# Kernel tuning notes

Hardware: AMD Instinct MI355X
Metric: run time of the kernel (lower is better)

## Reference

```python
import jax, jax.numpy as jnp
import numpy as np

B, T, J, C = 256, 100, 32, 3
EDGES = 101   # self.bins = bins + 1 edges
NBINS = EDGES - 1
EPS = 1e-08


def setup_inputs() -> dict:
    key = jax.random.key(0)
    k1, k2 = jax.random.split(key)
    data1 = jax.random.normal(k1, (B, T, J, C), dtype=jnp.float32)
    data2 = jax.random.normal(k2, (B, T, J, C), dtype=jnp.float32)
    return {"data1": data1, "data2": data2}


def _pairwise(d):
    # [B,T,J,C] -> [B,T,J,J] pairwise Euclidean distances over the joint axis
    diff = d[..., :, None, :] - d[..., None, :, :]
    return jnp.sqrt((diff * diff).sum(-1))


def _hist_density(x, edges):
    # x: [N] flat row, edges: [EDGES] sorted bin edges (torch.histogram semantics:
    # right-open bins, except the last bin which includes the right edge; density
    # normalizes by total count * bin width)
    idx = jnp.clip(jnp.searchsorted(edges, x, side='right') - 1, 0, NBINS - 1)
    counts = jnp.zeros(NBINS, dtype=x.dtype).at[idx].add(1.0)
    widths = jnp.diff(edges)
    return counts / (counts.sum() * widths)


def _entropy(px, qx):
    return (px * (jnp.log(px + EPS) - jnp.log(qx + EPS))).sum(1)


def reference(data1, data2):
    p1 = _pairwise(data1).reshape(data1.shape[0], -1)  # [B, T*J*J]
    p2 = _pairwise(data2).reshape(data2.shape[0], -1)
    both = jnp.concatenate([p1, p2], axis=1)
    mn = both.min(1)
    mx = both.max(1)
    # tensor_linspace: per-row uniform edges between row min and row max
    w0 = jnp.linspace(1.0, 0.0, EDGES, dtype=p1.dtype)
    w1 = jnp.linspace(0.0, 1.0, EDGES, dtype=p1.dtype)
    edges = mn[:, None] * w0 + mx[:, None] * w1  # [B, EDGES]
    px = jax.vmap(_hist_density)(p1, edges)  # [B, NBINS]
    qx = jax.vmap(_hist_density)(p2, edges)
    m = (px + qx) * 0.5
    return (_entropy(px, m) + _entropy(qx, m)) * 0.5  # [B]
```

## Files before the change

kernel.cpp:

```cpp
#include <hip/hip_runtime.h>

constexpr int BATCH       = 256;
constexpr int T           = 100;
constexpr int J           = 32;
constexpr int EDGES       = 101;
constexpr int NBINS       = 100;
constexpr int NPAIR       = (J * (J - 1)) / 2;
constexpr int PAIRS_TOTAL = T * NPAIR;
constexpr int NPOINTS     = T * J;
constexpr int ROW_FLOATS  = NPOINTS * 3;
constexpr int NREP        = 32;
constexpr int NTHREADS    = 1024;
constexpr int NWAVES      = NTHREADS / 64;
constexpr float EPSF      = 1e-8f;
constexpr float NTOT      = 102400.0f;

__device__ __forceinline__ float sqrt_approx(float s) {
    float r;
    asm("v_sqrt_f32 %0, %1" : "=v"(r) : "v"(s));
    return r;
}

__global__ __launch_bounds__(NTHREADS)
void jsd_kernel(const float* __restrict__ g1all,
                const float* __restrict__ g2all,
                float* __restrict__ out)
{
#pragma clang fp contract(off)
    __shared__ float2 spt[NPOINTS * 3];
    __shared__ unsigned int hist[2][NREP][EDGES];
    __shared__ unsigned int lut[NPAIR];
    __shared__ float edg[EDGES];
    __shared__ float sqe[EDGES];
    __shared__ float2 SQ2[NBINS];
    __shared__ float sred[NWAVES];
    __shared__ float sterm[NBINS];
    __shared__ float s_mx, s_invw;

    const int tid = threadIdx.x;
    const int row = blockIdx.x;
    const float* g1 = g1all + (size_t)row * ROW_FLOATS;
    const float* g2 = g2all + (size_t)row * ROW_FLOATS;

    for (int k = tid; k < NPOINTS; k += NTHREADS) {
        float x1 = g1[3 * k], y1 = g1[3 * k + 1], z1 = g1[3 * k + 2];
        float x2 = g2[3 * k], y2 = g2[3 * k + 1], z2 = g2[3 * k + 2];
        spt[3 * k + 0] = make_float2(x1, y1);
        spt[3 * k + 1] = make_float2(x2, y2);
        spt[3 * k + 2] = make_float2(z1, z2);
    }
    for (int k = tid; k < 2 * NREP * EDGES; k += NTHREADS)
        (&hist[0][0][0])[k] = 0u;
    if (tid < J) {
        const int a = tid;
        int p = a * (2 * J - a - 1) / 2;
        for (int c = a + 1; c < J; ++c)
            lut[p++] = (unsigned)(((a * 3) << 16) | (c * 3));
    }
    __syncthreads();

    float vmax = 0.0f;
    {
        int t0 = tid / NPAIR;
        int r  = tid - t0 * NPAIR;
        int tb = t0 * (J * 3);
        for (int p = tid; p < PAIRS_TOTAL; p += NTHREADS) {
            const unsigned e = lut[r];
            const int ia = tb + (int)(e >> 16);
            const int ib = tb + (int)(e & 0xffffu);
            float2 a0 = spt[ia], a1 = spt[ia + 1], a2 = spt[ia + 2];
            float2 b0 = spt[ib], b1 = spt[ib + 1], b2 = spt[ib + 2];
            float dx1 = a0.x - b0.x, dy1 = a0.y - b0.y, dz1 = a2.x - b2.x;
            float s1 = dx1 * dx1 + dy1 * dy1 + dz1 * dz1;
            float dx2 = a1.x - b1.x, dy2 = a1.y - b1.y, dz2 = a2.y - b2.y;
            float s2 = dx2 * dx2 + dy2 * dy2 + dz2 * dz2;
            vmax = fmaxf(vmax, fmaxf(s1, s2));
            r += 32;
            bool w = (r >= NPAIR);
            if (w) r -= NPAIR;
            tb += w ? (3 * J * 3) : (2 * J * 3);
        }
    }
    for (int off = 32; off > 0; off >>= 1)
        vmax = fmaxf(vmax, __shfl_down(vmax, off, 64));
    if ((tid & 63) == 0) sred[tid >> 6] = vmax;
    __syncthreads();
    if (tid == 0) {
        float m = sred[0];
        for (int w = 1; w < NWAVES; ++w) m = fmaxf(m, sred[w]);
        float mx = __fsqrt_rn(m);
        s_mx = mx;
        s_invw = 100.0f / mx;
    }
    __syncthreads();
    const float mx   = s_mx;
    const float invw = s_invw;

    if (tid < EDGES) {
        float w1 = (tid == EDGES - 1) ? 1.0f : ((float)tid * 0.01f);
        edg[tid] = mx * w1;
    }
    __syncthreads();

    if (tid < EDGES) {
        float e = edg[tid];
        float y = 0.0f;
        if (tid > 0) {
            y = __fmul_rn(e, e);
            for (int it = 0; it < 4 && __fsqrt_rn(y) < e; ++it)
                y = __int_as_float(__float_as_int(y) + 1);
            for (int it = 0; it < 8; ++it) {
                float py = __int_as_float(__float_as_int(y) - 1);
                if (__fsqrt_rn(py) >= e) y = py; else break;
            }
        }
        sqe[tid] = y;
    }
    __syncthreads();
    if (tid < NBINS) SQ2[tid] = make_float2(sqe[tid], sqe[tid + 1]);
    __syncthreads();

    const int rep = tid & (NREP - 1);
    unsigned int* __restrict__ h1 = &hist[0][rep][0];
    unsigned int* __restrict__ h2 = &hist[1][rep][0];
    {
        int t0 = tid / NPAIR;
        int r  = tid - t0 * NPAIR;
        int tb = t0 * (J * 3);
        for (int p = tid; p < PAIRS_TOTAL; p += NTHREADS) {
            const unsigned e = lut[r];
            const int ia = tb + (int)(e >> 16);
            const int ib = tb + (int)(e & 0xffffu);
            float2 a0 = spt[ia], a1 = spt[ia + 1], a2 = spt[ia + 2];
            float2 b0 = spt[ib], b1 = spt[ib + 1], b2 = spt[ib + 2];
            float dx1 = a0.x - b0.x, dy1 = a0.y - b0.y, dz1 = a2.x - b2.x;
            float s1 = dx1 * dx1 + dy1 * dy1 + dz1 * dz1;
            float dx2 = a1.x - b1.x, dy2 = a1.y - b1.y, dz2 = a2.y - b2.y;
            float s2 = dx2 * dx2 + dy2 * dy2 + dz2 * dz2;

            int i1 = (int)(sqrt_approx(s1) * invw);
            int i2 = (int)(sqrt_approx(s2) * invw);
            i1 = i1 < 0 ? 0 : (i1 > 99 ? 99 : i1);
            i2 = i2 < 0 ? 0 : (i2 > 99 ? 99 : i2);
            float2 t1 = SQ2[i1];
            float2 t2 = SQ2[i2];
            i1 += (s1 >= t1.y) ? 1 : 0;
            i1 -= (s1 <  t1.x) ? 1 : 0;
            i2 += (s2 >= t2.y) ? 1 : 0;
            i2 -= (s2 <  t2.x) ? 1 : 0;
            i1 = i1 > 99 ? 99 : i1;
            i2 = i2 > 99 ? 99 : i2;

            atomicAdd(&h1[i1], 2u);
            atomicAdd(&h2[i2], 2u);

            r += 32;
            bool w = (r >= NPAIR);
            if (w) r -= NPAIR;
            tb += w ? (3 * J * 3) : (2 * J * 3);
        }
    }
    __syncthreads();

    if (tid < NBINS) {
        unsigned int c1 = 0, c2 = 0;
        for (int rr = 0; rr < NREP; ++rr) { c1 += hist[0][rr][tid]; c2 += hist[1][rr][tid]; }
        if (tid == 0) { c1 += T * J; c2 += T * J; }

        float w   = edg[tid + 1] - edg[tid];
        float den = __fmul_rn(NTOT, w);
        float px  = __fdiv_rn((float)c1, den);
        float qx  = __fdiv_rn((float)c2, den);
        float m   = (px + qx) * 0.5f;
        float lm  = logf(m + EPSF);
        float term = px * (logf(px + EPSF) - lm) + qx * (logf(qx + EPSF) - lm);
        sterm[tid] = term;
    }
    __syncthreads();
    if (tid == 0) {
        float acc = 0.0f;
        for (int i = 0; i < NBINS; ++i) acc += sterm[i];
        out[row] = acc * 0.5f;
    }
}

extern "C" void kernel_launch(void* const* d_in, const int* in_sizes, int n_in,
                              void* d_out, int out_size, void* d_ws, size_t ws_size,
                              hipStream_t stream) {
    const float* d1 = (const float*)d_in[0];
    const float* d2 = (const float*)d_in[1];
    float* out = (float*)d_out;
    jsd_kernel<<<BATCH, NTHREADS, 0, stream>>>(d1, d2, out);
}
```

Measured before the change: 40.51 us.

## Restructure pairwise loop as circulant per-lane walk with register-held anchor joint

Replaces the LUT-indexed flat pair enumeration with a scheme where each lane owns one joint of a frame and walks offsets 1..16 cyclically. The offset-16 pairs are seen twice and get weight 1. The anchor joint's coordinates stay in registers and the LUT is removed. Shared memory uses a padded frame stride of 97 to reduce bank conflicts, and each lane's histogram replica is indexed by its joint. This is meant to cut LDS traffic and index arithmetic, at the cost of a tail pass for the last 4 frames and a fixed mapping of waves to frames.

```diff
diff --git a/kernel.cpp b/kernel.cpp
--- a/kernel.cpp
+++ b/kernel.cpp
@@ -1,19 +1,19 @@
 #include <hip/hip_runtime.h>
 
-constexpr int BATCH       = 256;
-constexpr int T           = 100;
-constexpr int J           = 32;
-constexpr int EDGES       = 101;
-constexpr int NBINS       = 100;
-constexpr int NPAIR       = (J * (J - 1)) / 2;
-constexpr int PAIRS_TOTAL = T * NPAIR;
-constexpr int NPOINTS     = T * J;
-constexpr int ROW_FLOATS  = NPOINTS * 3;
-constexpr int NREP        = 32;
-constexpr int NTHREADS    = 1024;
-constexpr int NWAVES      = NTHREADS / 64;
-constexpr float EPSF      = 1e-8f;
-constexpr float NTOT      = 102400.0f;
+constexpr int BATCH      = 256;
+constexpr int T          = 100;
+constexpr int J          = 32;
+constexpr int EDGES      = 101;
+constexpr int NBINS      = 100;
+constexpr int NPOINTS    = T * J;
+constexpr int ROW_FLOATS = NPOINTS * 3;
+constexpr int NREP       = 32;
+constexpr int NTHREADS   = 1024;
+constexpr int NWAVES     = NTHREADS / 64;
+constexpr int TSTRIDE    = 97;
+constexpr int TMAIN      = 96;
+constexpr float EPSF     = 1e-8f;
+constexpr float NTOT     = 102400.0f;
 
 __device__ __forceinline__ float sqrt_approx(float s) {
     float r;
@@ -27,9 +27,8 @@
                 float* __restrict__ out)
 {
 #pragma clang fp contract(off)
-    __shared__ float2 spt[NPOINTS * 3];
+    __shared__ float2 spt[T * TSTRIDE];
     __shared__ unsigned int hist[2][NREP][EDGES];
-    __shared__ unsigned int lut[NPAIR];
     __shared__ float edg[EDGES];
     __shared__ float sqe[EDGES];
     __shared__ float2 SQ2[NBINS];
@@ -37,53 +36,71 @@
     __shared__ float sterm[NBINS];
     __shared__ float s_mx, s_invw;
 
-    const int tid = threadIdx.x;
-    const int row = blockIdx.x;
+    const int tid  = threadIdx.x;
+    const int row  = blockIdx.x;
+    const int wid  = tid >> 6;
+    const int lane = tid & 63;
+    const int half = lane >> 5;
+    const int a    = lane & 31;
+    const int aoff = a * 3;
+
     const float* g1 = g1all + (size_t)row * ROW_FLOATS;
     const float* g2 = g2all + (size_t)row * ROW_FLOATS;
 
     for (int k = tid; k < NPOINTS; k += NTHREADS) {
         float x1 = g1[3 * k], y1 = g1[3 * k + 1], z1 = g1[3 * k + 2];
         float x2 = g2[3 * k], y2 = g2[3 * k + 1], z2 = g2[3 * k + 2];
-        spt[3 * k + 0] = make_float2(x1, y1);
-        spt[3 * k + 1] = make_float2(x2, y2);
-        spt[3 * k + 2] = make_float2(z1, z2);
+        const int base = (k >> 5) * TSTRIDE + (k & 31) * 3;
+        spt[base + 0] = make_float2(x1, y1);
+        spt[base + 1] = make_float2(x2, y2);
+        spt[base + 2] = make_float2(z1, z2);
     }
     for (int k = tid; k < 2 * NREP * EDGES; k += NTHREADS)
         (&hist[0][0][0])[k] = 0u;
-    if (tid < J) {
-        const int a = tid;
-        int p = a * (2 * J - a - 1) / 2;
-        for (int c = a + 1; c < J; ++c)
-            lut[p++] = (unsigned)(((a * 3) << 16) | (c * 3));
-    }
     __syncthreads();
 
     float vmax = 0.0f;
-    {
-        int t0 = tid / NPAIR;
-        int r  = tid - t0 * NPAIR;
-        int tb = t0 * (J * 3);
-        for (int p = tid; p < PAIRS_TOTAL; p += NTHREADS) {
-            const unsigned e = lut[r];
-            const int ia = tb + (int)(e >> 16);
-            const int ib = tb + (int)(e & 0xffffu);
-            float2 a0 = spt[ia], a1 = spt[ia + 1], a2 = spt[ia + 2];
-            float2 b0 = spt[ib], b1 = spt[ib + 1], b2 = spt[ib + 2];
-            float dx1 = a0.x - b0.x, dy1 = a0.y - b0.y, dz1 = a2.x - b2.x;
+    for (int r = 0; r < TMAIN / (NWAVES * 2); ++r) {
+        const int t    = r * (NWAVES * 2) + wid * 2 + half;
+        const int base = t * TSTRIDE;
+        const float2 o0 = spt[base + aoff];
+        const float2 o1 = spt[base + aoff + 1];
+        const float2 o2 = spt[base + aoff + 2];
+#pragma unroll 4
+        for (int k = 1; k <= 16; ++k) {
+            const int coff = base + ((a + k) & 31) * 3;
+            const float2 c0 = spt[coff];
+            const float2 c1 = spt[coff + 1];
+            const float2 c2 = spt[coff + 2];
+            float dx1 = o0.x - c0.x, dy1 = o0.y - c0.y, dz1 = o2.x - c2.x;
             float s1 = dx1 * dx1 + dy1 * dy1 + dz1 * dz1;
-            float dx2 = a1.x - b1.x, dy2 = a1.y - b1.y, dz2 = a2.y - b2.y;
+            float dx2 = o1.x - c1.x, dy2 = o1.y - c1.y, dz2 = o2.y - c2.y;
             float s2 = dx2 * dx2 + dy2 * dy2 + dz2 * dz2;
             vmax = fmaxf(vmax, fmaxf(s1, s2));
-            r += 32;
-            bool w = (r >= NPAIR);
-            if (w) r -= NPAIR;
-            tb += w ? (3 * J * 3) : (2 * J * 3);
         }
+    }
+#pragma unroll
+    for (int j = 0; j < 2; ++j) {
+        const int it   = wid * 4 + j * 2 + half;
+        const int t    = TMAIN + (it >> 4);
+        const int k    = (it & 15) + 1;
+        const int base = t * TSTRIDE;
+        const float2 o0 = spt[base + aoff];
+        const float2 o1 = spt[base + aoff + 1];
+        const float2 o2 = spt[base + aoff + 2];
+        const int coff = base + ((a + k) & 31) * 3;
+        const float2 c0 = spt[coff];
+        const float2 c1 = spt[coff + 1];
+        const float2 c2 = spt[coff + 2];
+        float dx1 = o0.x - c0.x, dy1 = o0.y - c0.y, dz1 = o2.x - c2.x;
+        float s1 = dx1 * dx1 + dy1 * dy1 + dz1 * dz1;
+        float dx2 = o1.x - c1.x, dy2 = o1.y - c1.y, dz2 = o2.y - c2.y;
+        float s2 = dx2 * dx2 + dy2 * dy2 + dz2 * dz2;
+        vmax = fmaxf(vmax, fmaxf(s1, s2));
     }
     for (int off = 32; off > 0; off >>= 1)
         vmax = fmaxf(vmax, __shfl_down(vmax, off, 64));
-    if ((tid & 63) == 0) sred[tid >> 6] = vmax;
+    if (lane == 0) sred[wid] = vmax;
     __syncthreads();
     if (tid == 0) {
         float m = sred[0];
@@ -93,12 +110,11 @@
         s_invw = 100.0f / mx;
     }
     __syncthreads();
-    const float mx   = s_mx;
     const float invw = s_invw;
 
     if (tid < EDGES) {
         float w1 = (tid == EDGES - 1) ? 1.0f : ((float)tid * 0.01f);
-        edg[tid] = mx * w1;
+        edg[tid] = s_mx * w1;
     }
     __syncthreads();
 
@@ -120,22 +136,23 @@
     if (tid < NBINS) SQ2[tid] = make_float2(sqe[tid], sqe[tid + 1]);
     __syncthreads();
 
-    const int rep = tid & (NREP - 1);
-    unsigned int* __restrict__ h1 = &hist[0][rep][0];
-    unsigned int* __restrict__ h2 = &hist[1][rep][0];
-    {
-        int t0 = tid / NPAIR;
-        int r  = tid - t0 * NPAIR;
-        int tb = t0 * (J * 3);
-        for (int p = tid; p < PAIRS_TOTAL; p += NTHREADS) {
-            const unsigned e = lut[r];
-            const int ia = tb + (int)(e >> 16);
-            const int ib = tb + (int)(e & 0xffffu);
-            float2 a0 = spt[ia], a1 = spt[ia + 1], a2 = spt[ia + 2];
-            float2 b0 = spt[ib], b1 = spt[ib + 1], b2 = spt[ib + 2];
-            float dx1 = a0.x - b0.x, dy1 = a0.y - b0.y, dz1 = a2.x - b2.x;
+    unsigned int* __restrict__ h1 = &hist[0][a][0];
+    unsigned int* __restrict__ h2 = &hist[1][a][0];
+    for (int r = 0; r < TMAIN / (NWAVES * 2); ++r) {
+        const int t    = r * (NWAVES * 2) + wid * 2 + half;
+        const int base = t * TSTRIDE;
+        const float2 o0 = spt[base + aoff];
+        const float2 o1 = spt[base + aoff + 1];
+        const float2 o2 = spt[base + aoff + 2];
+#pragma unroll 4
+        for (int k = 1; k <= 16; ++k) {
+            const int coff = base + ((a + k) & 31) * 3;
+            const float2 c0 = spt[coff];
+            const float2 c1 = spt[coff + 1];
+            const float2 c2 = spt[coff + 2];
+            float dx1 = o0.x - c0.x, dy1 = o0.y - c0.y, dz1 = o2.x - c2.x;
             float s1 = dx1 * dx1 + dy1 * dy1 + dz1 * dz1;
-            float dx2 = a1.x - b1.x, dy2 = a1.y - b1.y, dz2 = a2.y - b2.y;
+            float dx2 = o1.x - c1.x, dy2 = o1.y - c1.y, dz2 = o2.y - c2.y;
             float s2 = dx2 * dx2 + dy2 * dy2 + dz2 * dz2;
 
             int i1 = (int)(sqrt_approx(s1) * invw);
@@ -151,14 +168,45 @@
             i1 = i1 > 99 ? 99 : i1;
             i2 = i2 > 99 ? 99 : i2;
 
-            atomicAdd(&h1[i1], 2u);
-            atomicAdd(&h2[i2], 2u);
-
-            r += 32;
-            bool w = (r >= NPAIR);
-            if (w) r -= NPAIR;
-            tb += w ? (3 * J * 3) : (2 * J * 3);
+            const unsigned int wgt = (k < 16) ? 2u : 1u;
+            atomicAdd(&h1[i1], wgt);
+            atomicAdd(&h2[i2], wgt);
         }
+    }
+#pragma unroll
+    for (int j = 0; j < 2; ++j) {
+        const int it   = wid * 4 + j * 2 + half;
+        const int t    = TMAIN + (it >> 4);
+        const int k    = (it & 15) + 1;
+        const int base = t * TSTRIDE;
+        const float2 o0 = spt[base + aoff];
+        const float2 o1 = spt[base + aoff + 1];
+        const float2 o2 = spt[base + aoff + 2];
+        const int coff = base + ((a + k) & 31) * 3;
+        const float2 c0 = spt[coff];
+        const float2 c1 = spt[coff + 1];
+        const float2 c2 = spt[coff + 2];
+        float dx1 = o0.x - c0.x, dy1 = o0.y - c0.y, dz1 = o2.x - c2.x;
+        float s1 = dx1 * dx1 + dy1 * dy1 + dz1 * dz1;
+        float dx2 = o1.x - c1.x, dy2 = o1.y - c1.y, dz2 = o2.y - c2.y;
+        float s2 = dx2 * dx2 + dy2 * dy2 + dz2 * dz2;
+
+        int i1 = (int)(sqrt_approx(s1) * invw);
+        int i2 = (int)(sqrt_approx(s2) * invw);
+        i1 = i1 < 0 ? 0 : (i1 > 99 ? 99 : i1);
+        i2 = i2 < 0 ? 0 : (i2 > 99 ? 99 : i2);
+        float2 t1 = SQ2[i1];
+        float2 t2 = SQ2[i2];
+        i1 += (s1 >= t1.y) ? 1 : 0;
+        i1 -= (s1 <  t1.x) ? 1 : 0;
+        i2 += (s2 >= t2.y) ? 1 : 0;
+        i2 -= (s2 <  t2.x) ? 1 : 0;
+        i1 = i1 > 99 ? 99 : i1;
+        i2 = i2 > 99 ? 99 : i2;
+
+        const unsigned int wgt = (k < 16) ? 2u : 1u;
+        atomicAdd(&h1[i1], wgt);
+        atomicAdd(&h2[i2], wgt);
     }
     __syncthreads();
 
```

Measured after the change: 41.63 us. +2.8%, slower.

## Split JSD into max, histogram, and finalize kernels across time segments

Applied to the files above, without the earlier changes.

The single kernel that ran one 1024-thread block per batch row is split into three kernels. The first two each run 5 blocks per row (20 timesteps each), so the grid grows from 256 blocks to 1280. The max pass combines block results with a global atomicMax on the float bits. Partial histograms are summed into a global workspace with atomics, and a small third kernel computes the JSD. Pairs are now enumerated with a circular half-offset scheme that gives the diagonal-opposite pair weight 1, replacing the pair LUT. The design reloads the inputs twice and adds a memset and extra launches in exchange for more parallelism.

```diff
diff --git a/kernel.cpp b/kernel.cpp
--- a/kernel.cpp
+++ b/kernel.cpp
@@ -1,19 +1,21 @@
 #include <hip/hip_runtime.h>
 
-constexpr int BATCH       = 256;
-constexpr int T           = 100;
-constexpr int J           = 32;
-constexpr int EDGES       = 101;
-constexpr int NBINS       = 100;
-constexpr int NPAIR       = (J * (J - 1)) / 2;
-constexpr int PAIRS_TOTAL = T * NPAIR;
-constexpr int NPOINTS     = T * J;
-constexpr int ROW_FLOATS  = NPOINTS * 3;
-constexpr int NREP        = 32;
-constexpr int NTHREADS    = 1024;
-constexpr int NWAVES      = NTHREADS / 64;
-constexpr float EPSF      = 1e-8f;
-constexpr float NTOT      = 102400.0f;
+constexpr int BATCH      = 256;
+constexpr int T          = 100;
+constexpr int J          = 32;
+constexpr int EDGES      = 101;
+constexpr int NBINS      = 100;
+constexpr int ROW_FLOATS = T * J * 3;
+constexpr int TPB        = 20;
+constexpr int BPR        = 5;
+constexpr int NT1        = 640;
+constexpr int TSTRIDE    = 97;
+constexpr int NREP       = 32;
+constexpr float EPSF     = 1e-8f;
+constexpr float NTOT     = 102400.0f;
+
+constexpr size_t WS_HIST_OFF = 1024;
+constexpr size_t WS_BYTES    = WS_HIST_OFF + (size_t)BATCH * 2 * NBINS * sizeof(unsigned);
 
 __device__ __forceinline__ float sqrt_approx(float s) {
     float r;
@@ -21,65 +23,44 @@
     return r;
 }
 
-__global__ __launch_bounds__(NTHREADS)
-void jsd_kernel(const float* __restrict__ g1all,
-                const float* __restrict__ g2all,
-                float* __restrict__ out)
+__device__ __forceinline__ void stage_seg(float2* spt, const float* p1, const float* p2, int tid) {
+    const int t = tid >> 5, c = tid & 31;
+    const int base = t * TSTRIDE + c * 3;
+    spt[base + 0] = make_float2(p1[3 * tid],     p1[3 * tid + 1]);
+    spt[base + 1] = make_float2(p2[3 * tid],     p2[3 * tid + 1]);
+    spt[base + 2] = make_float2(p1[3 * tid + 2], p2[3 * tid + 2]);
+}
+
+__global__ __launch_bounds__(NT1)
+void k_max(const float* __restrict__ g1all, const float* __restrict__ g2all,
+           unsigned int* __restrict__ wmax)
 {
 #pragma clang fp contract(off)
-    __shared__ float2 spt[NPOINTS * 3];
-    __shared__ unsigned int hist[2][NREP][EDGES];
-    __shared__ unsigned int lut[NPAIR];
-    __shared__ float edg[EDGES];
-    __shared__ float sqe[EDGES];
-    __shared__ float2 SQ2[NBINS];
-    __shared__ float sred[NWAVES];
-    __shared__ float sterm[NBINS];
-    __shared__ float s_mx, s_invw;
-
-    const int tid = threadIdx.x;
-    const int row = blockIdx.x;
-    const float* g1 = g1all + (size_t)row * ROW_FLOATS;
-    const float* g2 = g2all + (size_t)row * ROW_FLOATS;
-
-    for (int k = tid; k < NPOINTS; k += NTHREADS) {
-        float x1 = g1[3 * k], y1 = g1[3 * k + 1], z1 = g1[3 * k + 2];
-        float x2 = g2[3 * k], y2 = g2[3 * k + 1], z2 = g2[3 * k + 2];
-        spt[3 * k + 0] = make_float2(x1, y1);
-        spt[3 * k + 1] = make_float2(x2, y2);
-        spt[3 * k + 2] = make_float2(z1, z2);
-    }
-    for (int k = tid; k < 2 * NREP * EDGES; k += NTHREADS)
-        (&hist[0][0][0])[k] = 0u;
-    if (tid < J) {
-        const int a = tid;
-        int p = a * (2 * J - a - 1) / 2;
-        for (int c = a + 1; c < J; ++c)
-            lut[p++] = (unsigned)(((a * 3) << 16) | (c * 3));
-    }
-    __syncthreads();
-
+    __shared__ float2 spt[TPB * TSTRIDE];
+    __shared__ float sred[NT1 / 64];
+    const int tid = threadIdx.x, bid = blockIdx.x;
+    const int row = bid / BPR, tseg = bid - row * BPR;
+    const float* p1 = g1all + (size_t)row * ROW_FLOATS + tseg * (TPB * J * 3);
+    const float* p2 = g2all + (size_t)row * ROW_FLOATS + tseg * (TPB * J * 3);
+
+    stage_seg(spt, p1, p2, tid);
+    __syncthreads();
+
+    const int hw = tid >> 5, a = tid & 31;
+    const int b = hw * TSTRIDE;
+    const float2 o0 = spt[b + a * 3];
+    const float2 o1 = spt[b + a * 3 + 1];
+    const float2 o2 = spt[b + a * 3 + 2];
     float vmax = 0.0f;
-    {
-        int t0 = tid / NPAIR;
-        int r  = tid - t0 * NPAIR;
-        int tb = t0 * (J * 3);
-        for (int p = tid; p < PAIRS_TOTAL; p += NTHREADS) {
-            const unsigned e = lut[r];
-            const int ia = tb + (int)(e >> 16);
-            const int ib = tb + (int)(e & 0xffffu);
-            float2 a0 = spt[ia], a1 = spt[ia + 1], a2 = spt[ia + 2];
-            float2 b0 = spt[ib], b1 = spt[ib + 1], b2 = spt[ib + 2];
-            float dx1 = a0.x - b0.x, dy1 = a0.y - b0.y, dz1 = a2.x - b2.x;
-            float s1 = dx1 * dx1 + dy1 * dy1 + dz1 * dz1;
-            float dx2 = a1.x - b1.x, dy2 = a1.y - b1.y, dz2 = a2.y - b2.y;
-            float s2 = dx2 * dx2 + dy2 * dy2 + dz2 * dz2;
-            vmax = fmaxf(vmax, fmaxf(s1, s2));
-            r += 32;
-            bool w = (r >= NPAIR);
-            if (w) r -= NPAIR;
-            tb += w ? (3 * J * 3) : (2 * J * 3);
-        }
+#pragma unroll 8
+    for (int k = 1; k <= 16; ++k) {
+        const int c = b + ((a + k) & 31) * 3;
+        const float2 c0 = spt[c], c1 = spt[c + 1], c2 = spt[c + 2];
+        float dx1 = o0.x - c0.x, dy1 = o0.y - c0.y, dz1 = o2.x - c2.x;
+        float s1 = dx1 * dx1 + dy1 * dy1 + dz1 * dz1;
+        float dx2 = o1.x - c1.x, dy2 = o1.y - c1.y, dz2 = o2.y - c2.y;
+        float s2 = dx2 * dx2 + dy2 * dy2 + dz2 * dz2;
+        vmax = fmaxf(vmax, fmaxf(s1, s2));
     }
     for (int off = 32; off > 0; off >>= 1)
         vmax = fmaxf(vmax, __shfl_down(vmax, off, 64));
@@ -87,23 +68,34 @@
     __syncthreads();
     if (tid == 0) {
         float m = sred[0];
-        for (int w = 1; w < NWAVES; ++w) m = fmaxf(m, sred[w]);
-        float mx = __fsqrt_rn(m);
-        s_mx = mx;
-        s_invw = 100.0f / mx;
-    }
-    __syncthreads();
-    const float mx   = s_mx;
-    const float invw = s_invw;
+        for (int w = 1; w < NT1 / 64; ++w) m = fmaxf(m, sred[w]);
+        atomicMax(&wmax[row], __float_as_uint(m));
+    }
+}
+
+__global__ __launch_bounds__(NT1)
+void k_hist(const float* __restrict__ g1all, const float* __restrict__ g2all,
+            const unsigned int* __restrict__ wmax, unsigned int* __restrict__ whist)
+{
+#pragma clang fp contract(off)
+    __shared__ float2 spt[TPB * TSTRIDE];
+    __shared__ unsigned int hist[2][NREP][EDGES];
+    __shared__ float sqe[EDGES];
+    __shared__ float2 SQ2[NBINS];
+    const int tid = threadIdx.x, bid = blockIdx.x;
+    const int row = bid / BPR, tseg = bid - row * BPR;
+    const float* p1 = g1all + (size_t)row * ROW_FLOATS + tseg * (TPB * J * 3);
+    const float* p2 = g2all + (size_t)row * ROW_FLOATS + tseg * (TPB * J * 3);
+
+    stage_seg(spt, p1, p2, tid);
+    for (int k = tid; k < 2 * NREP * EDGES; k += NT1)
+        (&hist[0][0][0])[k] = 0u;
+
+    const float mx   = __fsqrt_rn(__uint_as_float(wmax[row]));
+    const float invw = 100.0f / mx;
 
     if (tid < EDGES) {
-        float w1 = (tid == EDGES - 1) ? 1.0f : ((float)tid * 0.01f);
-        edg[tid] = mx * w1;
-    }
-    __syncthreads();
-
-    if (tid < EDGES) {
-        float e = edg[tid];
+        float e = (tid == EDGES - 1) ? mx : __fmul_rn(mx, __fmul_rn((float)tid, 0.01f));
         float y = 0.0f;
         if (tid > 0) {
             y = __fmul_rn(e, e);
@@ -120,51 +112,66 @@
     if (tid < NBINS) SQ2[tid] = make_float2(sqe[tid], sqe[tid + 1]);
     __syncthreads();
 
-    const int rep = tid & (NREP - 1);
-    unsigned int* __restrict__ h1 = &hist[0][rep][0];
-    unsigned int* __restrict__ h2 = &hist[1][rep][0];
-    {
-        int t0 = tid / NPAIR;
-        int r  = tid - t0 * NPAIR;
-        int tb = t0 * (J * 3);
-        for (int p = tid; p < PAIRS_TOTAL; p += NTHREADS) {
-            const unsigned e = lut[r];
-            const int ia = tb + (int)(e >> 16);
-            const int ib = tb + (int)(e & 0xffffu);
-            float2 a0 = spt[ia], a1 = spt[ia + 1], a2 = spt[ia + 2];
-            float2 b0 = spt[ib], b1 = spt[ib + 1], b2 = spt[ib + 2];
-            float dx1 = a0.x - b0.x, dy1 = a0.y - b0.y, dz1 = a2.x - b2.x;
-            float s1 = dx1 * dx1 + dy1 * dy1 + dz1 * dz1;
-            float dx2 = a1.x - b1.x, dy2 = a1.y - b1.y, dz2 = a2.y - b2.y;
-            float s2 = dx2 * dx2 + dy2 * dy2 + dz2 * dz2;
-
-            int i1 = (int)(sqrt_approx(s1) * invw);
-            int i2 = (int)(sqrt_approx(s2) * invw);
-            i1 = i1 < 0 ? 0 : (i1 > 99 ? 99 : i1);
-            i2 = i2 < 0 ? 0 : (i2 > 99 ? 99 : i2);
-            float2 t1 = SQ2[i1];
-            float2 t2 = SQ2[i2];
-            i1 += (s1 >= t1.y) ? 1 : 0;
-            i1 -= (s1 <  t1.x) ? 1 : 0;
-            i2 += (s2 >= t2.y) ? 1 : 0;
-            i2 -= (s2 <  t2.x) ? 1 : 0;
-            i1 = i1 > 99 ? 99 : i1;
-            i2 = i2 > 99 ? 99 : i2;
-
-            atomicAdd(&h1[i1], 2u);
-            atomicAdd(&h2[i2], 2u);
-
-            r += 32;
-            bool w = (r >= NPAIR);
-            if (w) r -= NPAIR;
-            tb += w ? (3 * J * 3) : (2 * J * 3);
-        }
-    }
-    __syncthreads();
-
+    const int hw = tid >> 5, a = tid & 31;
+    const int b = hw * TSTRIDE;
+    const float2 o0 = spt[b + a * 3];
+    const float2 o1 = spt[b + a * 3 + 1];
+    const float2 o2 = spt[b + a * 3 + 2];
+    unsigned int* __restrict__ h1 = &hist[0][a][0];
+    unsigned int* __restrict__ h2 = &hist[1][a][0];
+#pragma unroll 8
+    for (int k = 1; k <= 16; ++k) {
+        const int c = b + ((a + k) & 31) * 3;
+        const float2 c0 = spt[c], c1 = spt[c + 1], c2 = spt[c + 2];
+        float dx1 = o0.x - c0.x, dy1 = o0.y - c0.y, dz1 = o2.x - c2.x;
+        float s1 = dx1 * dx1 + dy1 * dy1 + dz1 * dz1;
+        float dx2 = o1.x - c1.x, dy2 = o1.y - c1.y, dz2 = o2.y - c2.y;
+        float s2 = dx2 * dx2 + dy2 * dy2 + dz2 * dz2;
+
+        int i1 = (int)(sqrt_approx(s1) * invw);
+        int i2 = (int)(sqrt_approx(s2) * invw);
+        i1 = i1 < 0 ? 0 : (i1 > 99 ? 99 : i1);
+        i2 = i2 < 0 ? 0 : (i2 > 99 ? 99 : i2);
+        float2 t1 = SQ2[i1];
+        float2 t2 = SQ2[i2];
+        i1 += (s1 >= t1.y) ? 1 : 0;
+        i1 -= (s1 <  t1.x) ? 1 : 0;
+        i2 += (s2 >= t2.y) ? 1 : 0;
+        i2 -= (s2 <  t2.x) ? 1 : 0;
+        i1 = i1 > 99 ? 99 : i1;
+        i2 = i2 > 99 ? 99 : i2;
+
+        const unsigned int wgt = (k < 16) ? 2u : 1u;
+        atomicAdd(&h1[i1], wgt);
+        atomicAdd(&h2[i2], wgt);
+    }
+    __syncthreads();
+
+    if (tid < 2 * NBINS) {
+        const int ds = tid / NBINS, bn = tid - ds * NBINS;
+        unsigned int s = 0;
+        for (int rr = 0; rr < NREP; ++rr) s += hist[ds][rr][bn];
+        atomicAdd(&whist[(row * 2 + ds) * NBINS + bn], s);
+    }
+}
+
+__global__ __launch_bounds__(128)
+void k_jsd(const unsigned int* __restrict__ wmax, const unsigned int* __restrict__ whist,
+           float* __restrict__ out)
+{
+#pragma clang fp contract(off)
+    __shared__ float edg[EDGES];
+    __shared__ float sterm[NBINS];
+    const int tid = threadIdx.x, row = blockIdx.x;
+    const float mx = __fsqrt_rn(__uint_as_float(wmax[row]));
+    if (tid < EDGES) {
+        float w1 = (tid == EDGES - 1) ? 1.0f : ((float)tid * 0.01f);
+        edg[tid] = mx * w1;
+    }
+    __syncthreads();
     if (tid < NBINS) {
-        unsigned int c1 = 0, c2 = 0;
-        for (int rr = 0; rr < NREP; ++rr) { c1 += hist[0][rr][tid]; c2 += hist[1][rr][tid]; }
+        unsigned int c1 = whist[(row * 2 + 0) * NBINS + tid];
+        unsigned int c2 = whist[(row * 2 + 1) * NBINS + tid];
         if (tid == 0) { c1 += T * J; c2 += T * J; }
 
         float w   = edg[tid + 1] - edg[tid];
@@ -173,8 +180,7 @@
         float qx  = __fdiv_rn((float)c2, den);
         float m   = (px + qx) * 0.5f;
         float lm  = logf(m + EPSF);
-        float term = px * (logf(px + EPSF) - lm) + qx * (logf(qx + EPSF) - lm);
-        sterm[tid] = term;
+        sterm[tid] = px * (logf(px + EPSF) - lm) + qx * (logf(qx + EPSF) - lm);
     }
     __syncthreads();
     if (tid == 0) {
@@ -190,5 +196,11 @@
     const float* d1 = (const float*)d_in[0];
     const float* d2 = (const float*)d_in[1];
     float* out = (float*)d_out;
-    jsd_kernel<<<BATCH, NTHREADS, 0, stream>>>(d1, d2, out);
-}
+    unsigned int* wmax  = (unsigned int*)d_ws;
+    unsigned int* whist = (unsigned int*)((char*)d_ws + WS_HIST_OFF);
+
+    hipMemsetAsync(d_ws, 0, WS_BYTES, stream);
+    k_max <<<BATCH * BPR, NT1, 0, stream>>>(d1, d2, wmax);
+    k_hist<<<BATCH * BPR, NT1, 0, stream>>>(d1, d2, wmax, whist);
+    k_jsd <<<BATCH, 128, 0, stream>>>(wmax, whist, out);
+}
```

Result: slower. 57.12 us (+41.0%).
